# Optimization experiments

Measured on AMD Instinct MI355X. Metric: run time of the kernel, lower is better.

The kernel has to match this reference:

```python
import jax, jax.numpy as jnp
import numpy as np

N = 4096
IN_DIM = 1433
HID = 64
OUT_DIM = 7
LAM_HAT = 0.9
LAM = 1.0 / LAM_HAT - 1.0          # skip-connection weight lambda
SCAD_A = 3.7
K_STEPS = 10
AVG_DEG = 32


def setup_inputs() -> dict:
    key = jax.random.key(0)
    k_a, k_x, k_w1, k_w2 = jax.random.split(key, 4)
    # symmetric binary adjacency, avg degree ~AVG_DEG, zero diagonal
    U = jax.random.uniform(k_a, (N, N), dtype=jnp.float32)
    p = AVG_DEG / N
    A = (jnp.minimum(U, U.T) < p).astype(jnp.float32)
    A = A * (1.0 - jnp.eye(N, dtype=jnp.float32))
    X = jax.random.normal(k_x, (N, IN_DIM), dtype=jnp.float32)
    w1 = jax.random.normal(k_w1, (IN_DIM, HID), dtype=jnp.float32) * (1.0 / np.sqrt(IN_DIM))
    b1 = jnp.zeros((HID,), dtype=jnp.float32)
    w2 = jax.random.normal(k_w2, (HID, OUT_DIM), dtype=jnp.float32) * (1.0 / np.sqrt(HID))
    b2 = jnp.zeros((OUT_DIM,), dtype=jnp.float32)
    log_gamma_0 = jnp.asarray(np.log(3.0), dtype=jnp.float32)          # gamma_0_init = 3.0
    raw_decay = jnp.asarray(np.log(0.85 / 0.15), dtype=jnp.float32)    # logit(0.85)
    return {"A": A, "X": X, "w1": w1, "b1": b1, "w2": w2, "b2": b2,
            "log_gamma_0": log_gamma_0, "raw_decay": raw_decay}


def _scad_weight(y, lam_k):
    """SCAD IRLS edge weight: 1 for y<=lam, linear roll-off to 0 at y=a*lam."""
    y_safe = jnp.maximum(y, 1e-12)  # avoid 0/0 in unselected branch
    w_mid = (SCAD_A * lam_k - y) / ((SCAD_A - 1.0) * y_safe)
    return jnp.where(y <= lam_k, 1.0,
                     jnp.where(y <= SCAD_A * lam_k, w_mid, 0.0))


def reference(A, X, w1, b1, w2, b2, log_gamma_0, raw_decay):
    # 1. MLP (eval mode: dropout = identity): X -> F0 in class space [N, C]
    F0 = jax.nn.relu(X @ w1 + b1) @ w2 + b2

    n = A.shape[0]
    eye = jnp.eye(n, dtype=A.dtype)
    A = A + eye                                   # add_loops
    D = A.sum(-1)                                 # [N]
    D_sq = jnp.sqrt(D)[:, None]                   # [N,1]
    d_is = 1.0 / jnp.sqrt(D)
    A_tilde = A * d_is[:, None] * d_is[None, :]   # sym_norm

    g0 = jnp.exp(log_gamma_0)
    r = jax.nn.sigmoid(raw_decay)

    F = F0
    for k in range(K_STEPS):
        gamma_k = g0 * (r ** k)
        lam_k = gamma_k / SCAD_A
        # pairwise squared Euclidean of degree-normalized features (detached)
        Fn = jax.lax.stop_gradient(F / D_sq)      # [N,C]
        sq = jnp.sum(Fn * Fn, axis=-1)
        Z = jnp.maximum(sq[:, None] + sq[None, :] - 2.0 * (Fn @ Fn.T), 0.0)
        y = jnp.sqrt(Z)                           # [N,N]
        W = _scad_weight(y, lam_k)
        W = W * (1.0 - eye)                       # zero diagonal
        W = jnp.where(jnp.isnan(W), 1.0, W)       # NaN guard (as in torch code)
        Q_hat = ((W * A).sum(-1) / D + LAM)[:, None]   # [N,1]
        F = (W * A_tilde) @ F / Q_hat + LAM * F0 / Q_hat
    return F


if __name__ == "__main__":
    out = reference(**setup_inputs())
    print(out.shape, out.dtype)
```

## Files before the change

kernel.cpp:

```cpp
#include <hip/hip_runtime.h>
#include <math.h>

#define N_NODES 4096
#define IN_DIM  1433
#define HID     64
#define OUT_DIM 7
#define FPAD    8
#define CAP     128
#define BR      64
#define KT      32

static constexpr float LAMBDA = (float)(1.0 / 0.9 - 1.0);
static constexpr float SCADA  = 3.7f;

__global__ __launch_bounds__(256) void build_adj(const float* __restrict__ A,
    int* __restrict__ nbr, int* __restrict__ cnt, float* __restrict__ deg,
    float* __restrict__ rsd) {
  int i = blockIdx.x;
  __shared__ int c;
  if (threadIdx.x == 0) c = 0;
  __syncthreads();
  const float4* row = (const float4*)(A + (size_t)i * N_NODES);
  for (int q = threadIdx.x; q < N_NODES / 4; q += 256) {
    float4 v = row[q];
    int j0 = q * 4;
    if (v.x != 0.0f) { int s = atomicAdd(&c, 1); if (s < CAP) nbr[(size_t)i * CAP + s] = j0; }
    if (v.y != 0.0f) { int s = atomicAdd(&c, 1); if (s < CAP) nbr[(size_t)i * CAP + s] = j0 + 1; }
    if (v.z != 0.0f) { int s = atomicAdd(&c, 1); if (s < CAP) nbr[(size_t)i * CAP + s] = j0 + 2; }
    if (v.w != 0.0f) { int s = atomicAdd(&c, 1); if (s < CAP) nbr[(size_t)i * CAP + s] = j0 + 3; }
  }
  __syncthreads();
  if (threadIdx.x == 0) {
    int cc = c; if (cc > CAP) cc = CAP;
    cnt[i] = cc;
    float d = (float)c + 1.0f;
    deg[i] = d;
    rsd[i] = 1.0f / sqrtf(d);
  }
}

__global__ __launch_bounds__(256) void gemm1(const float* __restrict__ X,
    const float* __restrict__ w1, float* __restrict__ P, int ksplit) {
  __shared__ __align__(16) float Xs[KT][BR + 4];
  __shared__ __align__(16) float Ws[KT][HID];
  const int t  = threadIdx.x;
  const int r0 = blockIdx.x * BR;
  const int ks = blockIdx.y;
  const int kbeg = (IN_DIM * ks) / ksplit;
  const int kend = (IN_DIM * (ks + 1)) / ksplit;
  const int rg = t >> 4;
  const int cg = t & 15;

  float acc[4][4];
  #pragma unroll
  for (int r = 0; r < 4; ++r)
    #pragma unroll
    for (int c = 0; c < 4; ++c) acc[r][c] = 0.0f;

  for (int k0 = kbeg; k0 < kend; k0 += KT) {
    #pragma unroll
    for (int j = 0; j < (BR * KT) / 256; ++j) {
      int e = t + 256 * j;
      int row = e >> 5;
      int kk  = e & (KT - 1);
      int k   = k0 + kk;
      float v = (k < kend) ? X[(size_t)(r0 + row) * IN_DIM + k] : 0.0f;
      Xs[kk][row] = v;
    }
    #pragma unroll
    for (int j = 0; j < (HID * KT) / 256; ++j) {
      int e = t + 256 * j;
      int kk  = e >> 6;
      int col = e & 63;
      int k   = k0 + kk;
      Ws[kk][col] = (k < kend) ? w1[(size_t)k * HID + col] : 0.0f;
    }
    __syncthreads();
    #pragma unroll
    for (int kk = 0; kk < KT; ++kk) {
      const float4 xv = *(const float4*)&Xs[kk][rg * 4];
      const float4 wv = *(const float4*)&Ws[kk][cg * 4];
      float xr[4] = {xv.x, xv.y, xv.z, xv.w};
      float wc[4] = {wv.x, wv.y, wv.z, wv.w};
      #pragma unroll
      for (int r = 0; r < 4; ++r)
        #pragma unroll
        for (int c = 0; c < 4; ++c) acc[r][c] += xr[r] * wc[c];
    }
    __syncthreads();
  }
  float* Pp = P + (size_t)ks * N_NODES * HID;
  #pragma unroll
  for (int r = 0; r < 4; ++r) {
    int row = r0 + rg * 4 + r;
    float4 v = make_float4(acc[r][0], acc[r][1], acc[r][2], acc[r][3]);
    *(float4*)&Pp[(size_t)row * HID + cg * 4] = v;
  }
}

__global__ __launch_bounds__(256) void reduce_h(const float* __restrict__ P,
    float* __restrict__ H, int ksplit) {
  int idx4 = blockIdx.x * 256 + threadIdx.x;
  const float4* P4 = (const float4*)P;
  float4 s = P4[idx4];
  for (int ks = 1; ks < ksplit; ++ks) {
    float4 v = P4[(size_t)ks * (N_NODES * HID / 4) + idx4];
    s.x += v.x; s.y += v.y; s.z += v.z; s.w += v.w;
  }
  ((float4*)H)[idx4] = s;
}

__global__ __launch_bounds__(256) void mlp_out(const float* __restrict__ H,
    const float* __restrict__ b1, const float* __restrict__ w2,
    const float* __restrict__ b2, float* __restrict__ F0, float* __restrict__ Fcur) {
  int t = blockIdx.x * blockDim.x + threadIdx.x;
  if (t >= N_NODES * FPAD) return;
  int row = t >> 3, c = t & 7;
  if (c == 7) { F0[t] = 0.0f; Fcur[t] = 0.0f; return; }
  float acc = b2[c];
  const float* h = H + (size_t)row * HID;
  #pragma unroll
  for (int k = 0; k < HID; ++k) {
    float hv = fmaxf(h[k] + b1[k], 0.0f);
    acc += hv * w2[k * OUT_DIM + c];
  }
  F0[t] = acc;
  Fcur[t] = acc;
}

__global__ __launch_bounds__(256) void rung_step(const float* __restrict__ Fin,
    const float* __restrict__ F0, float* __restrict__ Fout,
    const int* __restrict__ nbr, const int* __restrict__ cnt,
    const float* __restrict__ deg, const float* __restrict__ rsd,
    const float* __restrict__ lg0p, const float* __restrict__ rdp,
    int kstep, int last) {
  int wave = threadIdx.x >> 6;
  int lane = threadIdx.x & 63;
  int i = blockIdx.x * 4 + wave;

  float r_ = 1.0f / (1.0f + expf(-rdp[0]));
  float rk = 1.0f;
  for (int q = 0; q < kstep; ++q) rk *= r_;
  float lam = expf(lg0p[0]) * rk * (1.0f / SCADA);

  float rsi = rsd[i];
  float Di  = deg[i];
  int   ci  = cnt[i];
  float Fni[FPAD];
  {
    const float4* fp = (const float4*)(Fin + (size_t)i * FPAD);
    float4 a0 = fp[0], a1 = fp[1];
    Fni[0] = a0.x * rsi; Fni[1] = a0.y * rsi; Fni[2] = a0.z * rsi; Fni[3] = a0.w * rsi;
    Fni[4] = a1.x * rsi; Fni[5] = a1.y * rsi; Fni[6] = a1.z * rsi; Fni[7] = a1.w * rsi;
  }
  float s = 0.0f;
  float acc[FPAD] = {0, 0, 0, 0, 0, 0, 0, 0};
  for (int l = lane; l < ci; l += 64) {
    int j = nbr[(size_t)i * CAP + l];
    float rsj = rsd[j];
    const float4* fp = (const float4*)(Fin + (size_t)j * FPAD);
    float4 b0 = fp[0], b1v = fp[1];
    float fj[FPAD] = {b0.x, b0.y, b0.z, b0.w, b1v.x, b1v.y, b1v.z, b1v.w};
    float d2 = 0.0f;
    #pragma unroll
    for (int c = 0; c < FPAD; ++c) {
      float df = Fni[c] - fj[c] * rsj;
      d2 += df * df;
    }
    float y = sqrtf(d2);
    float w;
    if (y <= lam)              w = 1.0f;
    else if (y <= SCADA * lam) w = (SCADA * lam - y) / ((SCADA - 1.0f) * fmaxf(y, 1e-12f));
    else                       w = 0.0f;
    if (w != w) w = 1.0f;
    s += w;
    float wr = w * rsi * rsj;
    #pragma unroll
    for (int c = 0; c < FPAD; ++c) acc[c] += wr * fj[c];
  }
  #pragma unroll
  for (int off = 32; off > 0; off >>= 1) {
    s += __shfl_down(s, off);
    #pragma unroll
    for (int c = 0; c < FPAD; ++c) acc[c] += __shfl_down(acc[c], off);
  }
  if (lane == 0) {
    float Q = s / Di + LAMBDA;
    float inv = 1.0f / Q;
    if (last) {
      #pragma unroll
      for (int c = 0; c < OUT_DIM; ++c)
        Fout[(size_t)i * OUT_DIM + c] = (acc[c] + LAMBDA * F0[(size_t)i * FPAD + c]) * inv;
    } else {
      float o[FPAD];
      #pragma unroll
      for (int c = 0; c < FPAD; ++c)
        o[c] = (acc[c] + LAMBDA * F0[(size_t)i * FPAD + c]) * inv;
      float4* op = (float4*)(Fout + (size_t)i * FPAD);
      op[0] = make_float4(o[0], o[1], o[2], o[3]);
      op[1] = make_float4(o[4], o[5], o[6], o[7]);
    }
  }
}

extern "C" void kernel_launch(void* const* d_in, const int* in_sizes, int n_in,
                              void* d_out, int out_size, void* d_ws, size_t ws_size,
                              hipStream_t stream) {
  const float* A   = (const float*)d_in[0];
  const float* X   = (const float*)d_in[1];
  const float* w1  = (const float*)d_in[2];
  const float* b1  = (const float*)d_in[3];
  const float* w2  = (const float*)d_in[4];
  const float* b2  = (const float*)d_in[5];
  const float* lg0 = (const float*)d_in[6];
  const float* rd  = (const float*)d_in[7];
  float* out = (float*)d_out;

  const size_t fixed = (size_t)N_NODES * CAP * sizeof(int)
                     + (size_t)N_NODES * sizeof(int)
                     + (size_t)N_NODES * sizeof(float) * 2
                     + (size_t)N_NODES * HID * sizeof(float)
                     + (size_t)N_NODES * FPAD * sizeof(float) * 3;
  const size_t pbuf = (size_t)N_NODES * HID * sizeof(float);
  int ksplit = (ws_size >= fixed + 16 * pbuf) ? 16 : 8;

  char* w = (char*)d_ws;
  int*   nbr = (int*)w;   w += (size_t)N_NODES * CAP * sizeof(int);
  int*   cnt = (int*)w;   w += (size_t)N_NODES * sizeof(int);
  float* deg = (float*)w; w += (size_t)N_NODES * sizeof(float);
  float* rsd = (float*)w; w += (size_t)N_NODES * sizeof(float);
  float* P   = (float*)w; w += (size_t)ksplit * N_NODES * HID * sizeof(float);
  float* H   = (float*)w; w += (size_t)N_NODES * HID * sizeof(float);
  float* F0  = (float*)w; w += (size_t)N_NODES * FPAD * sizeof(float);
  float* FA  = (float*)w; w += (size_t)N_NODES * FPAD * sizeof(float);
  float* FB  = (float*)w; w += (size_t)N_NODES * FPAD * sizeof(float);

  build_adj<<<N_NODES, 256, 0, stream>>>(A, nbr, cnt, deg, rsd);
  gemm1<<<dim3(N_NODES / BR, ksplit), 256, 0, stream>>>(X, w1, P, ksplit);
  reduce_h<<<(N_NODES * HID / 4) / 256, 256, 0, stream>>>(P, H, ksplit);
  mlp_out<<<(N_NODES * FPAD) / 256, 256, 0, stream>>>(H, b1, w2, b2, F0, FA);

  float* cur = FA;
  float* nxt = FB;
  for (int k = 0; k < 10; ++k) {
    int last = (k == 9);
    float* dst = last ? out : nxt;
    rung_step<<<N_NODES / 4, 256, 0, stream>>>(cur, F0, dst, nbr, cnt, deg, rsd,
                                               lg0, rd, k, last);
    float* tmp = cur; cur = nxt; nxt = tmp;
  }
}
```

Measured before the change: 210.4 us.

## Fuse ten propagation steps into one cooperative kernel with grid syncs

Replaces the ten separate rung_step launches with one cooperative kernel that loops over the steps and calls grid.sync between them. Each node now uses a 32-lane sub-wave instead of a 64-lane wave, and neighbor indices and degree factors are loaded into registers once and reused across all steps. The intent is to remove launch overhead and repeated neighbor-list loads. In exchange it relies on cooperative launch of 512 blocks being co-resident, adds grid-sync cost per step, and assumes each node has at most 128 neighbors.

```diff
diff --git a/kernel.cpp b/kernel.cpp
--- a/kernel.cpp
+++ b/kernel.cpp
@@ -1,5 +1,8 @@
 #include <hip/hip_runtime.h>
+#include <hip/hip_cooperative_groups.h>
 #include <math.h>
+
+namespace cg = cooperative_groups;
 
 #define N_NODES 4096
 #define IN_DIM  1433
@@ -128,77 +131,103 @@
   Fcur[t] = acc;
 }
 
-__global__ __launch_bounds__(256) void rung_step(const float* __restrict__ Fin,
-    const float* __restrict__ F0, float* __restrict__ Fout,
+__global__ __launch_bounds__(256) void rung_fused(const float* __restrict__ F0,
+    float* __restrict__ FA, float* __restrict__ FB, float* __restrict__ out,
     const int* __restrict__ nbr, const int* __restrict__ cnt,
     const float* __restrict__ deg, const float* __restrict__ rsd,
-    const float* __restrict__ lg0p, const float* __restrict__ rdp,
-    int kstep, int last) {
-  int wave = threadIdx.x >> 6;
-  int lane = threadIdx.x & 63;
-  int i = blockIdx.x * 4 + wave;
-
-  float r_ = 1.0f / (1.0f + expf(-rdp[0]));
+    const float* __restrict__ lg0p, const float* __restrict__ rdp) {
+  cg::grid_group grid = cg::this_grid();
+  const int lane = threadIdx.x & 31;
+  const int i = (blockIdx.x * 256 + threadIdx.x) >> 5;
+
+  const float r_ = 1.0f / (1.0f + expf(-rdp[0]));
+  const float g0 = expf(lg0p[0]);
+  const float rsi = rsd[i];
+  const float Di  = deg[i];
+  const int   ci  = cnt[i];
+
+  int   j0 = 0, j1 = 0, j2 = 0, j3 = 0;
+  float q0 = 0.f, q1 = 0.f, q2 = 0.f, q3 = 0.f;
+  bool  e0 = (lane      < ci), e1 = (lane + 32 < ci),
+        e2 = (lane + 64 < ci), e3 = (lane + 96 < ci);
+  if (e0) { j0 = nbr[(size_t)i * CAP + lane     ]; q0 = rsd[j0]; }
+  if (e1) { j1 = nbr[(size_t)i * CAP + lane + 32]; q1 = rsd[j1]; }
+  if (e2) { j2 = nbr[(size_t)i * CAP + lane + 64]; q2 = rsd[j2]; }
+  if (e3) { j3 = nbr[(size_t)i * CAP + lane + 96]; q3 = rsd[j3]; }
+
+  const float* cur = FA;
+  float*       nxt = FB;
   float rk = 1.0f;
-  for (int q = 0; q < kstep; ++q) rk *= r_;
-  float lam = expf(lg0p[0]) * rk * (1.0f / SCADA);
-
-  float rsi = rsd[i];
-  float Di  = deg[i];
-  int   ci  = cnt[i];
-  float Fni[FPAD];
-  {
-    const float4* fp = (const float4*)(Fin + (size_t)i * FPAD);
-    float4 a0 = fp[0], a1 = fp[1];
-    Fni[0] = a0.x * rsi; Fni[1] = a0.y * rsi; Fni[2] = a0.z * rsi; Fni[3] = a0.w * rsi;
-    Fni[4] = a1.x * rsi; Fni[5] = a1.y * rsi; Fni[6] = a1.z * rsi; Fni[7] = a1.w * rsi;
-  }
-  float s = 0.0f;
-  float acc[FPAD] = {0, 0, 0, 0, 0, 0, 0, 0};
-  for (int l = lane; l < ci; l += 64) {
-    int j = nbr[(size_t)i * CAP + l];
-    float rsj = rsd[j];
-    const float4* fp = (const float4*)(Fin + (size_t)j * FPAD);
-    float4 b0 = fp[0], b1v = fp[1];
-    float fj[FPAD] = {b0.x, b0.y, b0.z, b0.w, b1v.x, b1v.y, b1v.z, b1v.w};
-    float d2 = 0.0f;
-    #pragma unroll
-    for (int c = 0; c < FPAD; ++c) {
-      float df = Fni[c] - fj[c] * rsj;
-      d2 += df * df;
-    }
-    float y = sqrtf(d2);
-    float w;
-    if (y <= lam)              w = 1.0f;
-    else if (y <= SCADA * lam) w = (SCADA * lam - y) / ((SCADA - 1.0f) * fmaxf(y, 1e-12f));
-    else                       w = 0.0f;
-    if (w != w) w = 1.0f;
-    s += w;
-    float wr = w * rsi * rsj;
-    #pragma unroll
-    for (int c = 0; c < FPAD; ++c) acc[c] += wr * fj[c];
-  }
-  #pragma unroll
-  for (int off = 32; off > 0; off >>= 1) {
-    s += __shfl_down(s, off);
-    #pragma unroll
-    for (int c = 0; c < FPAD; ++c) acc[c] += __shfl_down(acc[c], off);
-  }
-  if (lane == 0) {
-    float Q = s / Di + LAMBDA;
-    float inv = 1.0f / Q;
-    if (last) {
+
+  for (int k = 0; k < 10; ++k) {
+    const float lam = g0 * rk * (1.0f / SCADA);
+    rk *= r_;
+
+    const float4* fpi = (const float4*)(cur + (size_t)i * FPAD);
+    float4 a0 = fpi[0], a1 = fpi[1];
+    float Fni[FPAD] = {a0.x * rsi, a0.y * rsi, a0.z * rsi, a0.w * rsi,
+                       a1.x * rsi, a1.y * rsi, a1.z * rsi, a1.w * rsi};
+
+    float s = 0.0f;
+    float acc[FPAD] = {0, 0, 0, 0, 0, 0, 0, 0};
+
+    #define EDGE(EN, JN, QN)                                                  \
+    if (EN) {                                                                 \
+      const float4* fp = (const float4*)(cur + (size_t)(JN) * FPAD);          \
+      float4 b0 = fp[0], b1v = fp[1];                                         \
+      float fj[FPAD] = {b0.x, b0.y, b0.z, b0.w, b1v.x, b1v.y, b1v.z, b1v.w};  \
+      float d2 = 0.0f;                                                        \
+      _Pragma("unroll")                                                       \
+      for (int c = 0; c < FPAD; ++c) {                                        \
+        float df = Fni[c] - fj[c] * (QN);                                     \
+        d2 += df * df;                                                        \
+      }                                                                       \
+      float y = sqrtf(d2);                                                    \
+      float w;                                                                \
+      if (y <= lam)              w = 1.0f;                                    \
+      else if (y <= SCADA * lam) w = (SCADA * lam - y) /                      \
+                                     ((SCADA - 1.0f) * fmaxf(y, 1e-12f));     \
+      else                       w = 0.0f;                                    \
+      if (w != w) w = 1.0f;                                                   \
+      s += w;                                                                 \
+      float wr = w * rsi * (QN);                                              \
+      _Pragma("unroll")                                                       \
+      for (int c = 0; c < FPAD; ++c) acc[c] += wr * fj[c];                    \
+    }
+    EDGE(e0, j0, q0)
+    EDGE(e1, j1, q1)
+    EDGE(e2, j2, q2)
+    EDGE(e3, j3, q3)
+    #undef EDGE
+
+    #pragma unroll
+    for (int off = 16; off > 0; off >>= 1) {
+      s += __shfl_xor(s, off, 32);
       #pragma unroll
-      for (int c = 0; c < OUT_DIM; ++c)
-        Fout[(size_t)i * OUT_DIM + c] = (acc[c] + LAMBDA * F0[(size_t)i * FPAD + c]) * inv;
+      for (int c = 0; c < FPAD; ++c) acc[c] += __shfl_xor(acc[c], off, 32);
+    }
+
+    if (k == 9) {
+      if (lane == 0) {
+        float inv = 1.0f / (s / Di + LAMBDA);
+        #pragma unroll
+        for (int c = 0; c < OUT_DIM; ++c)
+          out[(size_t)i * OUT_DIM + c] =
+              (acc[c] + LAMBDA * F0[(size_t)i * FPAD + c]) * inv;
+      }
     } else {
-      float o[FPAD];
-      #pragma unroll
-      for (int c = 0; c < FPAD; ++c)
-        o[c] = (acc[c] + LAMBDA * F0[(size_t)i * FPAD + c]) * inv;
-      float4* op = (float4*)(Fout + (size_t)i * FPAD);
-      op[0] = make_float4(o[0], o[1], o[2], o[3]);
-      op[1] = make_float4(o[4], o[5], o[6], o[7]);
+      if (lane == 0) {
+        float inv = 1.0f / (s / Di + LAMBDA);
+        float o[FPAD];
+        #pragma unroll
+        for (int c = 0; c < FPAD; ++c)
+          o[c] = (acc[c] + LAMBDA * F0[(size_t)i * FPAD + c]) * inv;
+        float4* op = (float4*)(nxt + (size_t)i * FPAD);
+        op[0] = make_float4(o[0], o[1], o[2], o[3]);
+        op[1] = make_float4(o[4], o[5], o[6], o[7]);
+      }
+      grid.sync();
+      const float* tmp = cur; cur = nxt; nxt = (float*)tmp;
     }
   }
 }
@@ -240,13 +269,9 @@
   reduce_h<<<(N_NODES * HID / 4) / 256, 256, 0, stream>>>(P, H, ksplit);
   mlp_out<<<(N_NODES * FPAD) / 256, 256, 0, stream>>>(H, b1, w2, b2, F0, FA);
 
-  float* cur = FA;
-  float* nxt = FB;
-  for (int k = 0; k < 10; ++k) {
-    int last = (k == 9);
-    float* dst = last ? out : nxt;
-    rung_step<<<N_NODES / 4, 256, 0, stream>>>(cur, F0, dst, nbr, cnt, deg, rsd,
-                                               lg0, rd, k, last);
-    float* tmp = cur; cur = nxt; nxt = tmp;
-  }
-}
+  void* args[] = {(void*)&F0, (void*)&FA, (void*)&FB, (void*)&out,
+                  (void*)&nbr, (void*)&cnt, (void*)&deg, (void*)&rsd,
+                  (void*)&lg0, (void*)&rd};
+  hipLaunchCooperativeKernel((void*)rung_fused, dim3(N_NODES / 8), dim3(256),
+                             args, 0, stream);
+}
```

New measurement: 624.8 us. 197% more time.

## Use 16 lanes per node, pack neighbor index with degree scale, precompute lambdas

Applied to the files above, without the earlier changes.

The propagation kernel now gives each node 16 lanes instead of a full 64-lane wave, so four nodes share one wave and a degree of about 32 no longer leaves most lanes idle. A new pack_edges kernel stores each neighbor index together with its inverse-sqrt degree as an int2, removing one dependent gather per edge. The per-step lambda values are computed once in build_adj instead of recomputing exp and sigmoid in every thread. The cost is one extra kernel launch and extra workspace for the packed edge array.

```diff
diff --git a/kernel.cpp b/kernel.cpp
--- a/kernel.cpp
+++ b/kernel.cpp
@@ -9,14 +9,22 @@
 #define CAP     128
 #define BR      64
 #define KT      32
+#define LPN     16
 
 static constexpr float LAMBDA = (float)(1.0 / 0.9 - 1.0);
 static constexpr float SCADA  = 3.7f;
 
 __global__ __launch_bounds__(256) void build_adj(const float* __restrict__ A,
     int* __restrict__ nbr, int* __restrict__ cnt, float* __restrict__ deg,
-    float* __restrict__ rsd) {
+    float* __restrict__ rsd, float* __restrict__ lamt,
+    const float* __restrict__ lg0p, const float* __restrict__ rdp) {
   int i = blockIdx.x;
+  if (i == 0 && threadIdx.x == 0) {
+    float r_ = 1.0f / (1.0f + expf(-rdp[0]));
+    float g  = expf(lg0p[0]) * (1.0f / SCADA);
+    #pragma unroll
+    for (int k = 0; k < 10; ++k) { lamt[k] = g; g *= r_; }
+  }
   __shared__ int c;
   if (threadIdx.x == 0) c = 0;
   __syncthreads();
@@ -39,6 +47,17 @@
   }
 }
 
+__global__ __launch_bounds__(128) void pack_edges(const int* __restrict__ nbr,
+    const int* __restrict__ cnt, const float* __restrict__ rsd,
+    int2* __restrict__ ej) {
+  int i = blockIdx.x;
+  int s = threadIdx.x;
+  if (s < cnt[i]) {
+    int j = nbr[(size_t)i * CAP + s];
+    ej[(size_t)i * CAP + s] = make_int2(j, __float_as_int(rsd[j]));
+  }
+}
+
 __global__ __launch_bounds__(256) void gemm1(const float* __restrict__ X,
     const float* __restrict__ w1, float* __restrict__ P, int ksplit) {
   __shared__ __align__(16) float Xs[KT][BR + 4];
@@ -130,22 +149,17 @@
 
 __global__ __launch_bounds__(256) void rung_step(const float* __restrict__ Fin,
     const float* __restrict__ F0, float* __restrict__ Fout,
-    const int* __restrict__ nbr, const int* __restrict__ cnt,
+    const int2* __restrict__ ej, const int* __restrict__ cnt,
     const float* __restrict__ deg, const float* __restrict__ rsd,
-    const float* __restrict__ lg0p, const float* __restrict__ rdp,
-    int kstep, int last) {
-  int wave = threadIdx.x >> 6;
-  int lane = threadIdx.x & 63;
-  int i = blockIdx.x * 4 + wave;
-
-  float r_ = 1.0f / (1.0f + expf(-rdp[0]));
-  float rk = 1.0f;
-  for (int q = 0; q < kstep; ++q) rk *= r_;
-  float lam = expf(lg0p[0]) * rk * (1.0f / SCADA);
-
-  float rsi = rsd[i];
-  float Di  = deg[i];
-  int   ci  = cnt[i];
+    const float* __restrict__ lamt, int kstep, int last) {
+  const int lane = threadIdx.x & (LPN - 1);
+  const int i = (blockIdx.x * 256 + threadIdx.x) / LPN;
+
+  const float lam = lamt[kstep];
+  const float rsi = rsd[i];
+  const float Di  = deg[i];
+  const int   ci  = cnt[i];
+
   float Fni[FPAD];
   {
     const float4* fp = (const float4*)(Fin + (size_t)i * FPAD);
@@ -155,9 +169,11 @@
   }
   float s = 0.0f;
   float acc[FPAD] = {0, 0, 0, 0, 0, 0, 0, 0};
-  for (int l = lane; l < ci; l += 64) {
-    int j = nbr[(size_t)i * CAP + l];
-    float rsj = rsd[j];
+  const int2* ep = ej + (size_t)i * CAP;
+  for (int l = lane; l < ci; l += LPN) {
+    int2 e = ep[l];
+    int   j   = e.x;
+    float rsj = __int_as_float(e.y);
     const float4* fp = (const float4*)(Fin + (size_t)j * FPAD);
     float4 b0 = fp[0], b1v = fp[1];
     float fj[FPAD] = {b0.x, b0.y, b0.z, b0.w, b1v.x, b1v.y, b1v.z, b1v.w};
@@ -179,10 +195,10 @@
     for (int c = 0; c < FPAD; ++c) acc[c] += wr * fj[c];
   }
   #pragma unroll
-  for (int off = 32; off > 0; off >>= 1) {
-    s += __shfl_down(s, off);
-    #pragma unroll
-    for (int c = 0; c < FPAD; ++c) acc[c] += __shfl_down(acc[c], off);
+  for (int off = LPN / 2; off > 0; off >>= 1) {
+    s += __shfl_xor(s, off, LPN);
+    #pragma unroll
+    for (int c = 0; c < FPAD; ++c) acc[c] += __shfl_xor(acc[c], off, LPN);
   }
   if (lane == 0) {
     float Q = s / Di + LAMBDA;
@@ -219,8 +235,10 @@
   const size_t fixed = (size_t)N_NODES * CAP * sizeof(int)
                      + (size_t)N_NODES * sizeof(int)
                      + (size_t)N_NODES * sizeof(float) * 2
+                     + (size_t)N_NODES * CAP * sizeof(int2)
                      + (size_t)N_NODES * HID * sizeof(float)
-                     + (size_t)N_NODES * FPAD * sizeof(float) * 3;
+                     + (size_t)N_NODES * FPAD * sizeof(float) * 3
+                     + 64;
   const size_t pbuf = (size_t)N_NODES * HID * sizeof(float);
   int ksplit = (ws_size >= fixed + 16 * pbuf) ? 16 : 8;
 
@@ -229,13 +247,16 @@
   int*   cnt = (int*)w;   w += (size_t)N_NODES * sizeof(int);
   float* deg = (float*)w; w += (size_t)N_NODES * sizeof(float);
   float* rsd = (float*)w; w += (size_t)N_NODES * sizeof(float);
+  int2*  ej  = (int2*)w;  w += (size_t)N_NODES * CAP * sizeof(int2);
   float* P   = (float*)w; w += (size_t)ksplit * N_NODES * HID * sizeof(float);
   float* H   = (float*)w; w += (size_t)N_NODES * HID * sizeof(float);
   float* F0  = (float*)w; w += (size_t)N_NODES * FPAD * sizeof(float);
   float* FA  = (float*)w; w += (size_t)N_NODES * FPAD * sizeof(float);
   float* FB  = (float*)w; w += (size_t)N_NODES * FPAD * sizeof(float);
-
-  build_adj<<<N_NODES, 256, 0, stream>>>(A, nbr, cnt, deg, rsd);
+  float* lamt = (float*)w;
+
+  build_adj<<<N_NODES, 256, 0, stream>>>(A, nbr, cnt, deg, rsd, lamt, lg0, rd);
+  pack_edges<<<N_NODES, 128, 0, stream>>>(nbr, cnt, rsd, ej);
   gemm1<<<dim3(N_NODES / BR, ksplit), 256, 0, stream>>>(X, w1, P, ksplit);
   reduce_h<<<(N_NODES * HID / 4) / 256, 256, 0, stream>>>(P, H, ksplit);
   mlp_out<<<(N_NODES * FPAD) / 256, 256, 0, stream>>>(H, b1, w2, b2, F0, FA);
@@ -245,8 +266,8 @@
   for (int k = 0; k < 10; ++k) {
     int last = (k == 9);
     float* dst = last ? out : nxt;
-    rung_step<<<N_NODES / 4, 256, 0, stream>>>(cur, F0, dst, nbr, cnt, deg, rsd,
-                                               lg0, rd, k, last);
+    rung_step<<<(N_NODES * LPN) / 256, 256, 0, stream>>>(cur, F0, dst, ej, cnt,
+                                                         deg, rsd, lamt, k, last);
     float* tmp = cur; cur = nxt; nxt = tmp;
   }
 }
```

Measured after the change: 209.6 us. Within noise of the previous version (-0.4%).
